# Performance work log

Hardware: AMD Instinct MI355X
Metric: run time of the kernel (lower is better)

The kernel has to match this reference:

```python
import jax, jax.numpy as jnp
import numpy as np

NEG_SLOPE_ATT = 0.2   # DenseGATConv default negative_slope
NEG_SLOPE_OUT = 0.01  # F.leaky_relu default


def dense_gat_layer(x, adj, w, att_src, att_dst, bias, heads, concat):
    # x: [B, N, F_in], adj: [B, N, N] (0/1 float), w: [F_in, H*C]
    B, N, _ = x.shape
    h = (x @ w).reshape(B, N, heads, -1)                 # [B, N, H, C]
    a_src = jnp.einsum('bnhc,hc->bnh', h, att_src)       # [B, N, H]
    a_dst = jnp.einsum('bnhc,hc->bnh', h, att_dst)       # [B, N, H]
    # alpha[b,i,j,h] = a_src[b,j,h] + a_dst[b,i,h]
    alpha = a_src[:, None, :, :] + a_dst[:, :, None, :]  # [B, N, N, H]
    alpha = jax.nn.leaky_relu(alpha, NEG_SLOPE_ATT)
    alpha = jnp.where(adj[..., None] == 0, -jnp.inf, alpha)
    alpha = jax.nn.softmax(alpha, axis=2)                # over neighbors j
    out = jnp.einsum('bijh,bjhc->bihc', alpha, h)        # [B, N, H, C]
    if concat:
        out = out.reshape(B, N, -1)                      # [B, N, H*C]
    else:
        out = out.mean(axis=2)                           # [B, N, C]
    return out + bias


def setup_inputs() -> dict:
    key = jax.random.key(0)
    ks = jax.random.split(key, 9)
    B, N, F_IN, HID, H1, OUT = 1, 4096, 256, 64, 8, 128
    x = jax.random.normal(ks[0], (B, N, F_IN), dtype=jnp.float32)
    u = jax.random.uniform(ks[1], (B, N, N), dtype=jnp.float32)
    adj = (u < 0.05).astype(jnp.float32)
    eye = jnp.eye(N, dtype=jnp.float32)[None]
    adj = jnp.maximum(adj, eye)  # ensure self-loop so softmax rows are valid
    s1 = 1.0 / np.sqrt(F_IN)
    s2 = 1.0 / np.sqrt(HID * H1)
    return {
        'x': x,
        'adj': adj,
        'w1': jax.random.normal(ks[2], (F_IN, H1 * HID), dtype=jnp.float32) * s1,
        'att_src1': jax.random.normal(ks[3], (H1, HID), dtype=jnp.float32) * s2,
        'att_dst1': jax.random.normal(ks[4], (H1, HID), dtype=jnp.float32) * s2,
        'b1': jnp.zeros((H1 * HID,), dtype=jnp.float32),
        'w2': jax.random.normal(ks[5], (H1 * HID, OUT), dtype=jnp.float32) * s2,
        'att_src2': jax.random.normal(ks[6], (1, OUT), dtype=jnp.float32) * 0.1,
        'att_dst2': jax.random.normal(ks[7], (1, OUT), dtype=jnp.float32) * 0.1,
        'b2': jnp.zeros((OUT,), dtype=jnp.float32),
    }


def reference(x, adj, w1, att_src1, att_dst1, b1, w2, att_src2, att_dst2, b2):
    h = dense_gat_layer(x, adj, w1, att_src1, att_dst1, b1, heads=8, concat=True)
    h = jax.nn.leaky_relu(h, NEG_SLOPE_OUT)
    h = dense_gat_layer(h, adj, w2, att_src2, att_dst2, b2, heads=1, concat=False)
    return jax.nn.leaky_relu(h, NEG_SLOPE_OUT)
```

## Files before the change

kernel.cpp:

```cpp
#include <hip/hip_runtime.h>
#include <hip/hip_bf16.h>
#include <cstdint>

#define N_NODES 4096
#define STRIDE  384
#define NPAIRS_MAX 192
#define QMAX    128
#define WROW    400

typedef _Float16 half2v __attribute__((ext_vector_type(2)));
typedef _Float16 v4h __attribute__((ext_vector_type(4)));
typedef _Float16 v8h __attribute__((ext_vector_type(8)));
typedef float    v4f __attribute__((ext_vector_type(4)));
typedef unsigned u4v __attribute__((ext_vector_type(4)));

__device__ __forceinline__ float f16lo(unsigned u) {
    half2v h = __builtin_bit_cast(half2v, u); return (float)h.x;
}
__device__ __forceinline__ float f16hi(unsigned u) {
    half2v h = __builtin_bit_cast(half2v, u); return (float)h.y;
}
__device__ __forceinline__ unsigned pk_lo(unsigned a, unsigned b) {
    return __builtin_amdgcn_perm(b, a, 0x05040100u);
}
__device__ __forceinline__ unsigned pk_hi(unsigned a, unsigned b) {
    return __builtin_amdgcn_perm(b, a, 0x07060302u);
}
__device__ __forceinline__ float fdot2f(unsigned v, unsigned w, float acc) {
    return __builtin_amdgcn_fdot2(__builtin_bit_cast(half2v, v),
                                  __builtin_bit_cast(half2v, w), acc, false);
}
__device__ __forceinline__ float lrelu02(float s) { return (s > 0.f) ? s : 0.2f * s; }
__device__ __forceinline__ float lrelu01(float s) { return (s > 0.f) ? s : 0.01f * s; }

__global__ __launch_bounds__(256) void setup_kernel(
    const float* __restrict__ adj, unsigned short* __restrict__ nbr,
    int* __restrict__ cnt,
    const float* __restrict__ w1, const float* __restrict__ w2,
    _Float16* __restrict__ w1T, _Float16* __restrict__ w2T,
    float* __restrict__ as2, float* __restrict__ ad2) {
    const int b = blockIdx.x, t = threadIdx.x;
    if (b < 4096) {
        const int i    = b;
        const int wv   = t >> 6;
        const int lane = t & 63;
        __shared__ unsigned short s_buf[4][QMAX];
        __shared__ int s_cnt[4];
        const float4* row = (const float4*)(adj + (size_t)i * N_NODES);
        int base = 0;
#pragma unroll
        for (int it = 0; it < 4; it++) {
            float4 v = row[wv * 256 + it * 64 + lane];
            float e4[4] = {v.x, v.y, v.z, v.w};
            unsigned long long m4[4];
#pragma unroll
            for (int e = 0; e < 4; e++) m4[e] = __ballot(e4[e] != 0.0f);
#pragma unroll
            for (int e = 0; e < 4; e++) {
                int prefix = __popcll(m4[e] & ((1ull << lane) - 1ull));
                int pos = base + prefix;
                if (e4[e] != 0.0f && pos < QMAX)
                    s_buf[wv][pos] = (unsigned short)(wv * 1024 + (it * 64 + lane) * 4 + e);
                base += __popcll(m4[e]);
            }
        }
        if (lane == 0) s_cnt[wv] = (base < QMAX) ? base : QMAX;
        __syncthreads();
        const int c0 = s_cnt[0], c1 = s_cnt[1], c2 = s_cnt[2], c3 = s_cnt[3];
        const int o1 = c0, o2 = c0 + c1, o3 = o2 + c2;
        int total = o3 + c3;
        if (total > STRIDE) total = STRIDE;
        for (int k = t; k < total; k += 256) {
            int w, loc;
            if      (k < o1) { w = 0; loc = k; }
            else if (k < o2) { w = 1; loc = k - o1; }
            else if (k < o3) { w = 2; loc = k - o2; }
            else             { w = 3; loc = k - o3; }
            nbr[(size_t)i * STRIDE + k] = s_buf[w][loc];
        }
        if (t == 0) cnt[i] = total;
    } else if (b < 4608) {
        const int idx = (b - 4096) * 256 + t;
        const int n = idx >> 8, k = idx & 255;
        w1T[idx] = (_Float16)w1[k * 512 + n];
    } else if (b < 4768) {
        const int idx = (b - 4608) * 410;
        const int e   = idx + t;
        for (int q = e; q < idx + 410 && q < 65536; q += 256) {
            const int n = q >> 9, k = q & 511;
            w2T[q] = (_Float16)w2[k * 128 + n];
        }
    } else {
        const int idx = (b - 4768) * 256 + t;
        as2[idx] = 0.f;
        ad2[idx] = 0.f;
    }
}

template<int KCH, int NSUB, int H, bool AF32>
__global__ __launch_bounds__(256) void gemm_mfma_kernel(
    const void* __restrict__ Aptr, const _Float16* __restrict__ BT16,
    _Float16* __restrict__ C16,
    const float* __restrict__ att_s, const float* __restrict__ att_d,
    float* __restrict__ as_, float* __restrict__ ad_, int N) {
    const int K    = KCH * 32;
    const int wid  = blockIdx.x * 4 + (threadIdx.x >> 6);
    const int lane = threadIdx.x & 63;
    const int quad = lane >> 4, l16 = lane & 15;
    const int ntiles = N / (16 * NSUB);
    const int m0 = (wid / ntiles) * 16;
    const int n0 = (wid % ntiles) * (16 * NSUB);

    v8h a[KCH];
    if constexpr (AF32) {
        const float* ax = (const float*)Aptr + (size_t)(m0 + l16) * K + quad * 8;
#pragma unroll
        for (int c = 0; c < KCH; c++) {
            const float4 p = *(const float4*)(ax + c * 32);
            const float4 q = *(const float4*)(ax + c * 32 + 4);
            v8h h;
            h[0] = (_Float16)p.x; h[1] = (_Float16)p.y;
            h[2] = (_Float16)p.z; h[3] = (_Float16)p.w;
            h[4] = (_Float16)q.x; h[5] = (_Float16)q.y;
            h[6] = (_Float16)q.z; h[7] = (_Float16)q.w;
            a[c] = h;
        }
    } else {
        const v8h* arow = (const v8h*)((const _Float16*)Aptr +
                                       (size_t)(m0 + l16) * K + quad * 8);
#pragma unroll
        for (int c = 0; c < KCH; c++) a[c] = arow[c * 4];
    }

    float ps[4] = {}, pd[4] = {};
#pragma unroll
    for (int s = 0; s < NSUB; s++) {
        const int n = n0 + s * 16 + l16;
        const v8h* brow = (const v8h*)(BT16 + (size_t)n * K + quad * 8);
        v4f acc = {0.f, 0.f, 0.f, 0.f};
#pragma unroll
        for (int c = 0; c < KCH; c++)
            acc = __builtin_amdgcn_mfma_f32_16x16x32_f16(a[c], brow[c * 4], acc, 0, 0, 0);
        const float sa = att_s[n], sd = att_d[n];
#pragma unroll
        for (int r = 0; r < 4; r++) {
            C16[(size_t)(m0 + quad * 4 + r) * N + n] = (_Float16)acc[r];
            ps[r] += acc[r] * sa;
            pd[r] += acc[r] * sd;
        }
    }
#pragma unroll
    for (int r = 0; r < 4; r++) {
#pragma unroll
        for (int off = 1; off < 16; off <<= 1) {
            ps[r] += __shfl_xor(ps[r], off);
            pd[r] += __shfl_xor(pd[r], off);
        }
    }
    if (l16 == 0) {
#pragma unroll
        for (int r = 0; r < 4; r++) {
            const int row = m0 + quad * 4 + r;
            if (H > 1) {
                const int head = n0 >> 6;
                as_[row * H + head] = ps[r];
                ad_[row * H + head] = pd[r];
            } else {
                atomicAdd(&as_[row], ps[r]);
                atomicAdd(&ad_[row], pd[r]);
            }
        }
    }
}

__global__ __launch_bounds__(128) void attn1_kernel(
    const _Float16* __restrict__ h1g, const float* __restrict__ asrc,
    const float* __restrict__ adst, const unsigned short* __restrict__ nbr,
    const int* __restrict__ cnt, const float* __restrict__ b1,
    _Float16* __restrict__ out1f16) {
    const int i    = blockIdx.x;
    const int wv   = threadIdx.x >> 6;
    const int lane = threadIdx.x & 63;
    const int hd   = lane >> 3;
    __shared__ __align__(16) unsigned s_nb[NPAIRS_MAX];
    __shared__ __align__(16) unsigned short s_w16[8][WROW];
    __shared__ __align__(16) float s_comb[512];
    __shared__ float s_ml[2][2][8];

    const int n      = cnt[i];
    const int npairs = (n + 1) >> 1;
    const int nq     = (npairs + 3) >> 2;
    const int npadp  = nq * 4;
    const int npadE  = npadp * 2;

    const unsigned* nbr32 = (const unsigned*)(nbr + (size_t)i * STRIDE);
    for (int k0 = wv * 32; k0 < npadp; k0 += 128) {
        const int k = k0 + (lane & 31) + ((lane >= 32) ? 64 : 0);
        if (k < npadp) {
            unsigned v = 0u;
            if (2 * k + 1 < n)  v = nbr32[k];
            else if (2 * k < n) v = nbr32[k] & 0xffffu;
            s_nb[k] = v;
        }
    }

    float ad8[8];
    {
        const float4 a0 = *(const float4*)(adst + i * 8);
        const float4 a1 = *(const float4*)(adst + i * 8 + 4);
        ad8[0]=a0.x; ad8[1]=a0.y; ad8[2]=a0.z; ad8[3]=a0.w;
        ad8[4]=a1.x; ad8[5]=a1.y; ad8[6]=a1.z; ad8[7]=a1.w;
    }
    float m8[8];
#pragma unroll
    for (int k = 0; k < 8; k++) m8[k] = -1e30f;
    for (int e0 = wv * 64; e0 < n; e0 += 128) {
        const int e = e0 + lane;
        if (e < n) {
            const int id = (s_nb[e >> 1] >> ((e & 1) * 16)) & 0xffff;
            const float4 q0 = *(const float4*)(asrc + id * 8);
            const float4 q1 = *(const float4*)(asrc + id * 8 + 4);
            const float sv[8] = {q0.x, q0.y, q0.z, q0.w, q1.x, q1.y, q1.z, q1.w};
#pragma unroll
            for (int k = 0; k < 8; k++) m8[k] = fmaxf(m8[k], lrelu02(sv[k] + ad8[k]));
        }
    }
#pragma unroll
    for (int k = 0; k < 8; k++)
#pragma unroll
        for (int off = 32; off; off >>= 1) m8[k] = fmaxf(m8[k], __shfl_xor(m8[k], off));

    float l8[8];
#pragma unroll
    for (int k = 0; k < 8; k++) l8[k] = 0.f;
    for (int e0 = wv * 64; e0 < npadE; e0 += 128) {
        const int e = e0 + lane;
        if (e < n) {
            const int id = (s_nb[e >> 1] >> ((e & 1) * 16)) & 0xffff;
            const float4 q0 = *(const float4*)(asrc + id * 8);
            const float4 q1 = *(const float4*)(asrc + id * 8 + 4);
            const float sv[8] = {q0.x, q0.y, q0.z, q0.w, q1.x, q1.y, q1.z, q1.w};
#pragma unroll
            for (int k = 0; k < 8; k++) {
                float ev = __expf(lrelu02(sv[k] + ad8[k]) - m8[k]);
                _Float16 h = (_Float16)ev;
                l8[k] += (float)h;
                s_w16[k][e] = __builtin_bit_cast(unsigned short, h);
            }
        } else if (e < npadE) {
#pragma unroll
            for (int k = 0; k < 8; k++) s_w16[k][e] = 0;
        }
    }
#pragma unroll
    for (int k = 0; k < 8; k++)
#pragma unroll
        for (int off = 32; off; off >>= 1) l8[k] += __shfl_xor(l8[k], off);

    const char* hb = (const char*)h1g + lane * 16;
    const unsigned* wbase = (const unsigned*)&s_w16[hd][0];
    float ac[8] = {};
    for (int q0 = wv * 8; q0 < nq; q0 += 16) {
#pragma unroll
        for (int qq = 0; qq < 8; qq++) {
            const int q = q0 + qq;
            if (q >= nq) break;
            const uint4 idq = *(const uint4*)&s_nb[q * 4];
            const uint4 wq  = *(const uint4*)(wbase + q * 4);
            const unsigned idv[4] = {idq.x, idq.y, idq.z, idq.w};
            const unsigned wv4[4] = {wq.x, wq.y, wq.z, wq.w};
#pragma unroll
            for (int p = 0; p < 4; p++) {
                const int iA = idv[p] & 0xffff, iB = idv[p] >> 16;
                const uint4 vA = *(const uint4*)(hb + (size_t)iA * 1024);
                const uint4 vB = *(const uint4*)(hb + (size_t)iB * 1024);
                const unsigned w = wv4[p];
                ac[0] = fdot2f(pk_lo(vA.x, vB.x), w, ac[0]);
                ac[1] = fdot2f(pk_hi(vA.x, vB.x), w, ac[1]);
                ac[2] = fdot2f(pk_lo(vA.y, vB.y), w, ac[2]);
                ac[3] = fdot2f(pk_hi(vA.y, vB.y), w, ac[3]);
                ac[4] = fdot2f(pk_lo(vA.z, vB.z), w, ac[4]);
                ac[5] = fdot2f(pk_hi(vA.z, vB.z), w, ac[5]);
                ac[6] = fdot2f(pk_lo(vA.w, vB.w), w, ac[6]);
                ac[7] = fdot2f(pk_hi(vA.w, vB.w), w, ac[7]);
            }
        }
    }
    if (wv == 0) {
        *(float4*)&s_comb[lane * 8]     = make_float4(ac[0], ac[1], ac[2], ac[3]);
        *(float4*)&s_comb[lane * 8 + 4] = make_float4(ac[4], ac[5], ac[6], ac[7]);
    }
    if (lane == 0) {
#pragma unroll
        for (int k = 0; k < 8; k++) {
            s_ml[wv][0][k] = m8[k];
            s_ml[wv][1][k] = l8[k];
        }
    }
    __syncthreads();
    if (wv == 1) {
        const float m0v = s_ml[0][0][hd], l0v = s_ml[0][1][hd];
        const float m1v = s_ml[1][0][hd], l1v = s_ml[1][1][hd];
        const float mm = fmaxf(m0v, m1v);
        const float a0s = __expf(m0v - mm), a1s = __expf(m1v - mm);
        const float inv = 1.0f / (l0v * a0s + l1v * a1s);
        const float4 c0 = *(const float4*)&s_comb[lane * 8];
        const float4 c1 = *(const float4*)&s_comb[lane * 8 + 4];
        const float o8[8] = {
            c0.x * a0s + ac[0] * a1s, c0.y * a0s + ac[1] * a1s,
            c0.z * a0s + ac[2] * a1s, c0.w * a0s + ac[3] * a1s,
            c1.x * a0s + ac[4] * a1s, c1.y * a0s + ac[5] * a1s,
            c1.z * a0s + ac[6] * a1s, c1.w * a0s + ac[7] * a1s };
        const float4 bb0 = *(const float4*)(b1 + lane * 8);
        const float4 bb1 = *(const float4*)(b1 + lane * 8 + 4);
        const float bbv[8] = {bb0.x, bb0.y, bb0.z, bb0.w, bb1.x, bb1.y, bb1.z, bb1.w};
        v8h ov;
#pragma unroll
        for (int c = 0; c < 8; c++)
            ov[c] = (_Float16)lrelu01(o8[c] * inv + bbv[c]);
        *(v8h*)(out1f16 + (size_t)i * 512 + lane * 8) = ov;
    }
}

__global__ __launch_bounds__(128) void attn2_kernel(
    const _Float16* __restrict__ h2g, const float* __restrict__ asrc,
    const float* __restrict__ adst, const unsigned short* __restrict__ nbr,
    const int* __restrict__ cnt, const float* __restrict__ b2,
    float* __restrict__ out) {
    const int wv   = threadIdx.x >> 6;
    const int i    = blockIdx.x * 2 + wv;
    const int lane = threadIdx.x & 63;
    const int grp  = lane >> 4, l16 = lane & 15;
    __shared__ __align__(16) unsigned s_nb[2][NPAIRS_MAX];
    __shared__ __align__(16) unsigned short s_w16[2][STRIDE + 16];

    const int n     = cnt[i];
    const int nq4   = (n + 3) >> 2;
    const int npad4 = nq4 * 4;
    const int npadp = (npad4 + 1) >> 1;

    const unsigned* nbr32 = (const unsigned*)(nbr + (size_t)i * STRIDE);
    for (int k = lane; k < npadp; k += 64) {
        unsigned v = 0u;
        if (2 * k + 1 < n)  v = nbr32[k];
        else if (2 * k < n) v = nbr32[k] & 0xffffu;
        s_nb[wv][k] = v;
    }

    const float ad = adst[i];
    float sreg[6];
    float m = -1e30f;
#pragma unroll
    for (int it = 0; it < 6; it++) {
        const int e = it * 64 + lane;
        float s = -1e30f;
        if (e < n) {
            const int id = (s_nb[wv][e >> 1] >> ((e & 1) * 16)) & 0xffff;
            s = lrelu02(asrc[id] + ad);
        }
        sreg[it] = s;
        m = fmaxf(m, s);
    }
#pragma unroll
    for (int off = 32; off; off >>= 1) m = fmaxf(m, __shfl_xor(m, off));
    float l = 0.f;
#pragma unroll
    for (int it = 0; it < 6; it++) {
        const int e = it * 64 + lane;
        if (e < n) {
            float ev = __expf(sreg[it] - m);
            _Float16 h = (_Float16)ev;
            l += (float)h;
            s_w16[wv][e] = __builtin_bit_cast(unsigned short, h);
        }
    }
    if (lane < npad4 - n) s_w16[wv][n + lane] = 0;
#pragma unroll
    for (int off = 32; off; off >>= 1) l += __shfl_xor(l, off);
    const float inv = 1.0f / l;

    const char* hb = (const char*)h2g + l16 * 16;
    float ac[8] = {};
    for (int it = 0; it < nq4; it++) {
        const int e = it * 4 + grp;
        const unsigned pr = s_nb[wv][e >> 1];
        const int id = (e & 1) ? (int)(pr >> 16) : (int)(pr & 0xffffu);
        const float w = (float)((const _Float16*)&s_w16[wv][0])[e];
        const uint4 v = *(const uint4*)(hb + (size_t)id * 256);
        ac[0] += w * f16lo(v.x); ac[1] += w * f16hi(v.x);
        ac[2] += w * f16lo(v.y); ac[3] += w * f16hi(v.y);
        ac[4] += w * f16lo(v.z); ac[5] += w * f16hi(v.z);
        ac[6] += w * f16lo(v.w); ac[7] += w * f16hi(v.w);
    }
#pragma unroll
    for (int c = 0; c < 8; c++) {
        ac[c] += __shfl_xor(ac[c], 16);
        ac[c] += __shfl_xor(ac[c], 32);
    }
    if (lane < 16) {
        const float4 bb0 = *(const float4*)(b2 + lane * 8);
        const float4 bb1 = *(const float4*)(b2 + lane * 8 + 4);
        float4 o0, o1;
        o0.x = lrelu01(ac[0] * inv + bb0.x);
        o0.y = lrelu01(ac[1] * inv + bb0.y);
        o0.z = lrelu01(ac[2] * inv + bb0.z);
        o0.w = lrelu01(ac[3] * inv + bb0.w);
        o1.x = lrelu01(ac[4] * inv + bb1.x);
        o1.y = lrelu01(ac[5] * inv + bb1.y);
        o1.z = lrelu01(ac[6] * inv + bb1.z);
        o1.w = lrelu01(ac[7] * inv + bb1.w);
        *(float4*)(out + (size_t)i * 128 + lane * 8)     = o0;
        *(float4*)(out + (size_t)i * 128 + lane * 8 + 4) = o1;
    }
}

extern "C" void kernel_launch(void* const* d_in, const int* in_sizes, int n_in,
                              void* d_out, int out_size, void* d_ws, size_t ws_size,
                              hipStream_t stream) {
    const float* x        = (const float*)d_in[0];
    const float* adj      = (const float*)d_in[1];
    const float* w1       = (const float*)d_in[2];
    const float* att_src1 = (const float*)d_in[3];
    const float* att_dst1 = (const float*)d_in[4];
    const float* b1       = (const float*)d_in[5];
    const float* w2       = (const float*)d_in[6];
    const float* att_src2 = (const float*)d_in[7];
    const float* att_dst2 = (const float*)d_in[8];
    const float* b2       = (const float*)d_in[9];
    float* out = (float*)d_out;

    float* ws   = (float*)d_ws;
    float* as1  = ws;
    float* ad1  = as1 + 4096 * 8;
    float* as2  = ad1 + 4096 * 8;
    float* ad2  = as2 + 4096;
    int*   cnt  = (int*)(ad2 + 4096);
    _Float16* w1T   = (_Float16*)(cnt + 4096);
    _Float16* w2T   = w1T + 512 * 256;
    _Float16* h1g   = w2T + 128 * 512;
    _Float16* out1h = h1g + (size_t)4096 * 512;
    _Float16* h2g   = out1h + (size_t)4096 * 512;
    unsigned short* nbr = (unsigned short*)(h2g + (size_t)4096 * 128);

    setup_kernel<<<4784, 256, 0, stream>>>(adj, nbr, cnt, w1, w2,
                                           w1T, w2T, as2, ad2);

    gemm_mfma_kernel<8, 4, 8, true><<<512, 256, 0, stream>>>(
        x, w1T, h1g, att_src1, att_dst1, as1, ad1, 512);
    attn1_kernel<<<N_NODES, 128, 0, stream>>>(h1g, as1, ad1, nbr, cnt, b1, out1h);

    gemm_mfma_kernel<16, 2, 1, false><<<256, 256, 0, stream>>>(
        out1h, w2T, h2g, att_src2, att_dst2, as2, ad2, 128);
    attn2_kernel<<<N_NODES / 2, 128, 0, stream>>>(h2g, as2, ad2, nbr, cnt, b2, out);
}
```

Measured before the change: 194.9 us.

## Overlap adjacency compaction with first GEMM in one combined kernel launch

The adjacency compaction moves out of the setup kernel and into a new combined kernel. The first 512 blocks of that kernel run the layer-1 MFMA GEMM and the remaining 4096 blocks build the neighbor lists. Weight transposes and the zeroing of as2/ad2 go into a smaller prep kernel. The aim is to let the bandwidth-bound 64MB adjacency scan run alongside the compute-bound GEMM instead of before it. The cost is a heterogeneous grid whose block scheduling and resource limits are set by the GEMM path.

Result: slower. 199.0 us (+2.1%).

```diff
diff --git a/kernel.cpp b/kernel.cpp
--- a/kernel.cpp
+++ b/kernel.cpp
@@ -12,7 +12,6 @@
 typedef _Float16 v4h __attribute__((ext_vector_type(4)));
 typedef _Float16 v8h __attribute__((ext_vector_type(8)));
 typedef float    v4f __attribute__((ext_vector_type(4)));
-typedef unsigned u4v __attribute__((ext_vector_type(4)));
 
 __device__ __forceinline__ float f16lo(unsigned u) {
     half2v h = __builtin_bit_cast(half2v, u); return (float)h.x;
@@ -33,15 +32,92 @@
 __device__ __forceinline__ float lrelu02(float s) { return (s > 0.f) ? s : 0.2f * s; }
 __device__ __forceinline__ float lrelu01(float s) { return (s > 0.f) ? s : 0.01f * s; }
 
-__global__ __launch_bounds__(256) void setup_kernel(
-    const float* __restrict__ adj, unsigned short* __restrict__ nbr,
-    int* __restrict__ cnt,
+__global__ __launch_bounds__(256) void prep_kernel(
     const float* __restrict__ w1, const float* __restrict__ w2,
     _Float16* __restrict__ w1T, _Float16* __restrict__ w2T,
     float* __restrict__ as2, float* __restrict__ ad2) {
     const int b = blockIdx.x, t = threadIdx.x;
-    if (b < 4096) {
-        const int i    = b;
+    if (b < 512) {
+        const int idx = b * 256 + t;
+        const int n = idx >> 8, k = idx & 255;
+        w1T[idx] = (_Float16)w1[k * 512 + n];
+    } else if (b < 672) {
+        const int idx = (b - 512) * 410;
+        for (int q = idx + t; q < idx + 410 && q < 65536; q += 256) {
+            const int n = q >> 9, k = q & 511;
+            w2T[q] = (_Float16)w2[k * 128 + n];
+        }
+    } else {
+        const int idx = (b - 672) * 256 + t;
+        as2[idx] = 0.f;
+        ad2[idx] = 0.f;
+    }
+}
+
+__global__ __launch_bounds__(256) void gemm1_compact_kernel(
+    const float* __restrict__ x, const _Float16* __restrict__ w1T,
+    _Float16* __restrict__ C16,
+    const float* __restrict__ att_s, const float* __restrict__ att_d,
+    float* __restrict__ as_, float* __restrict__ ad_,
+    const float* __restrict__ adj, unsigned short* __restrict__ nbr,
+    int* __restrict__ cnt) {
+    if (blockIdx.x < 512) {
+        const int wid  = blockIdx.x * 4 + (threadIdx.x >> 6);
+        const int lane = threadIdx.x & 63;
+        const int quad = lane >> 4, l16 = lane & 15;
+        const int m0 = (wid >> 3) * 16;
+        const int n0 = (wid & 7) * 64;
+
+        v8h a[8];
+        const float* ax = x + (size_t)(m0 + l16) * 256 + quad * 8;
+#pragma unroll
+        for (int c = 0; c < 8; c++) {
+            const float4 p = *(const float4*)(ax + c * 32);
+            const float4 q = *(const float4*)(ax + c * 32 + 4);
+            v8h h;
+            h[0] = (_Float16)p.x; h[1] = (_Float16)p.y;
+            h[2] = (_Float16)p.z; h[3] = (_Float16)p.w;
+            h[4] = (_Float16)q.x; h[5] = (_Float16)q.y;
+            h[6] = (_Float16)q.z; h[7] = (_Float16)q.w;
+            a[c] = h;
+        }
+        float ps[4] = {}, pd[4] = {};
+#pragma unroll
+        for (int s = 0; s < 4; s++) {
+            const int n = n0 + s * 16 + l16;
+            const v8h* brow = (const v8h*)(w1T + (size_t)n * 256 + quad * 8);
+            v4f acc = {0.f, 0.f, 0.f, 0.f};
+#pragma unroll
+            for (int c = 0; c < 8; c++)
+                acc = __builtin_amdgcn_mfma_f32_16x16x32_f16(a[c], brow[c * 4], acc, 0, 0, 0);
+            const float sa = att_s[n], sd = att_d[n];
+#pragma unroll
+            for (int r = 0; r < 4; r++) {
+                C16[(size_t)(m0 + quad * 4 + r) * 512 + n] = (_Float16)acc[r];
+                ps[r] += acc[r] * sa;
+                pd[r] += acc[r] * sd;
+            }
+        }
+#pragma unroll
+        for (int r = 0; r < 4; r++) {
+#pragma unroll
+            for (int off = 1; off < 16; off <<= 1) {
+                ps[r] += __shfl_xor(ps[r], off);
+                pd[r] += __shfl_xor(pd[r], off);
+            }
+        }
+        if (l16 == 0) {
+            const int head = n0 >> 6;
+#pragma unroll
+            for (int r = 0; r < 4; r++) {
+                const int row = m0 + quad * 4 + r;
+                as_[row * 8 + head] = ps[r];
+                ad_[row * 8 + head] = pd[r];
+            }
+        }
+    } else {
+        const int i    = blockIdx.x - 512;
+        const int t    = threadIdx.x;
         const int wv   = t >> 6;
         const int lane = t & 63;
         __shared__ unsigned short s_buf[4][QMAX];
@@ -79,27 +155,12 @@
             nbr[(size_t)i * STRIDE + k] = s_buf[w][loc];
         }
         if (t == 0) cnt[i] = total;
-    } else if (b < 4608) {
-        const int idx = (b - 4096) * 256 + t;
-        const int n = idx >> 8, k = idx & 255;
-        w1T[idx] = (_Float16)w1[k * 512 + n];
-    } else if (b < 4768) {
-        const int idx = (b - 4608) * 410;
-        const int e   = idx + t;
-        for (int q = e; q < idx + 410 && q < 65536; q += 256) {
-            const int n = q >> 9, k = q & 511;
-            w2T[q] = (_Float16)w2[k * 128 + n];
-        }
-    } else {
-        const int idx = (b - 4768) * 256 + t;
-        as2[idx] = 0.f;
-        ad2[idx] = 0.f;
-    }
-}
-
-template<int KCH, int NSUB, int H, bool AF32>
+    }
+}
+
+template<int KCH, int NSUB, int H>
 __global__ __launch_bounds__(256) void gemm_mfma_kernel(
-    const void* __restrict__ Aptr, const _Float16* __restrict__ BT16,
+    const _Float16* __restrict__ A16, const _Float16* __restrict__ BT16,
     _Float16* __restrict__ C16,
     const float* __restrict__ att_s, const float* __restrict__ att_d,
     float* __restrict__ as_, float* __restrict__ ad_, int N) {
@@ -112,25 +173,9 @@
     const int n0 = (wid % ntiles) * (16 * NSUB);
 
     v8h a[KCH];
-    if constexpr (AF32) {
-        const float* ax = (const float*)Aptr + (size_t)(m0 + l16) * K + quad * 8;
-#pragma unroll
-        for (int c = 0; c < KCH; c++) {
-            const float4 p = *(const float4*)(ax + c * 32);
-            const float4 q = *(const float4*)(ax + c * 32 + 4);
-            v8h h;
-            h[0] = (_Float16)p.x; h[1] = (_Float16)p.y;
-            h[2] = (_Float16)p.z; h[3] = (_Float16)p.w;
-            h[4] = (_Float16)q.x; h[5] = (_Float16)q.y;
-            h[6] = (_Float16)q.z; h[7] = (_Float16)q.w;
-            a[c] = h;
-        }
-    } else {
-        const v8h* arow = (const v8h*)((const _Float16*)Aptr +
-                                       (size_t)(m0 + l16) * K + quad * 8);
-#pragma unroll
-        for (int c = 0; c < KCH; c++) a[c] = arow[c * 4];
-    }
+    const v8h* arow = (const v8h*)(A16 + (size_t)(m0 + l16) * K + quad * 8);
+#pragma unroll
+    for (int c = 0; c < KCH; c++) a[c] = arow[c * 4];
 
     float ps[4] = {}, pd[4] = {};
 #pragma unroll
@@ -442,14 +487,14 @@
     _Float16* h2g   = out1h + (size_t)4096 * 512;
     unsigned short* nbr = (unsigned short*)(h2g + (size_t)4096 * 128);
 
-    setup_kernel<<<4784, 256, 0, stream>>>(adj, nbr, cnt, w1, w2,
-                                           w1T, w2T, as2, ad2);
-
-    gemm_mfma_kernel<8, 4, 8, true><<<512, 256, 0, stream>>>(
-        x, w1T, h1g, att_src1, att_dst1, as1, ad1, 512);
+    prep_kernel<<<688, 256, 0, stream>>>(w1, w2, w1T, w2T, as2, ad2);
+
+    gemm1_compact_kernel<<<4608, 256, 0, stream>>>(
+        x, w1T, h1g, att_src1, att_dst1, as1, ad1, adj, nbr, cnt);
+
     attn1_kernel<<<N_NODES, 128, 0, stream>>>(h1g, as1, ad1, nbr, cnt, b1, out1h);
 
-    gemm_mfma_kernel<16, 2, 1, false><<<256, 256, 0, stream>>>(
+    gemm_mfma_kernel<16, 2, 1><<<256, 256, 0, stream>>>(
         out1h, w2T, h2g, att_src2, att_dst2, as2, ad2, 128);
     attn2_kernel<<<N_NODES / 2, 128, 0, stream>>>(h2g, as2, ad2, nbr, cnt, b2, out);
 }
```
